# Kernel optimization log

Hardware: AMD Instinct MI355X
Metric: run time of the kernel (lower is better)

## Reference

```python
import jax, jax.numpy as jnp
from jax import lax
import numpy as np

H = W = 32          # feature map size (1024px image / stride 32)
A = 9               # 3 scales x 3 ratios
IOU_THR = 0.5
DN = ('NCHW', 'OIHW', 'NCHW')


def _base_anchors():
    scales = [8.0, 16.0, 32.0]
    ratios = [0.5, 1.0, 2.0]
    rows = []
    for s in scales:
        for r in ratios:
            w = s * np.sqrt(r)
            h = s / np.sqrt(r)
            rows.append([-w / 2, -h / 2, w / 2, h / 2])
    return jnp.asarray(np.array(rows, dtype=np.float32))  # [A,4]


def setup_inputs() -> dict:
    key = jax.random.key(0)
    ks = jax.random.split(key, 4)
    x = jax.random.normal(ks[0], (1, 2048, H, W), jnp.float32)
    # small weight scale keeps exp(dw) in a sane range, like a trained RPN
    conv_w = jax.random.normal(ks[1], (512, 2048, 3, 3), jnp.float32) * 0.01
    conv_b = jnp.zeros((512,), jnp.float32)
    cls_w = jax.random.normal(ks[2], (2 * A, 512, 1, 1), jnp.float32) * 0.01
    cls_b = jnp.zeros((2 * A,), jnp.float32)
    bbox_w = jax.random.normal(ks[3], (4 * A, 512, 1, 1), jnp.float32) * 0.01
    bbox_b = jnp.zeros((4 * A,), jnp.float32)
    return {"x": x, "conv_w": conv_w, "conv_b": conv_b,
            "cls_w": cls_w, "cls_b": cls_b, "bbox_w": bbox_w, "bbox_b": bbox_b}


def _conv(x, w, b, pad):
    y = lax.conv_general_dilated(x, w, (1, 1), pad, dimension_numbers=DN)
    return y + b[None, :, None, None]


def _pairwise_iou(boxes):
    # boxes: [N,4] (x1,y1,x2,y2)
    area = (boxes[:, 2] - boxes[:, 0]) * (boxes[:, 3] - boxes[:, 1])
    lt = jnp.maximum(boxes[:, None, :2], boxes[None, :, :2])
    rb = jnp.minimum(boxes[:, None, 2:], boxes[None, :, 2:])
    wh = jnp.clip(rb - lt, 0.0)
    inter = wh[..., 0] * wh[..., 1]
    union = area[:, None] + area[None, :] - inter
    return inter / jnp.maximum(union, 1e-9)


def _nms_keep(boxes_sorted):
    # boxes sorted by descending score; sequential greedy suppression
    n = boxes_sorted.shape[0]
    iou = _pairwise_iou(boxes_sorted)  # [N,N]
    idx = jnp.arange(n)
    def body(i, keep):
        sup = (iou[i] > IOU_THR) & (idx > i) & keep[i]
        return keep & ~sup
    return lax.fori_loop(0, n, body, jnp.ones((n,), bool))


def _rpn_forward(x, conv_w, conv_b, cls_w, cls_b, bbox_w, bbox_b):
    feat = jax.nn.relu(_conv(x, conv_w, conv_b, 'SAME'))            # [1,512,H,W]
    obj = _conv(feat, cls_w, cls_b, 'VALID')                        # [1,18,H,W]
    deltas = _conv(feat, bbox_w, bbox_b, 'VALID')                   # [1,36,H,W]

    # softmax over the 2 classes (torch view(B,2,-1): first 9 channels = class 0)
    probs = jax.nn.softmax(obj[0].reshape(2, -1), axis=0)[1]        # [A*H*W] anchor-major
    scores = probs.reshape(A, H, W).transpose(1, 2, 0).reshape(-1)  # (pos, anchor) order

    # bbox channel layout: channel = a*4 + coord (0::4 slicing in torch)
    d = deltas[0].reshape(A, 4, H, W).transpose(2, 3, 0, 1).reshape(-1, 4)  # [N,4]

    anchors = jnp.tile(_base_anchors(), (H * W, 1))                 # [N,4], pos*9+a
    aw = anchors[:, 2] - anchors[:, 0]
    ah = anchors[:, 3] - anchors[:, 1]
    cx = anchors[:, 0] + 0.5 * aw
    cy = anchors[:, 1] + 0.5 * ah
    px = cx + d[:, 0] * aw
    py = cy + d[:, 1] * ah
    pw = jnp.exp(d[:, 2]) * aw
    ph = jnp.exp(d[:, 3]) * ah
    boxes = jnp.stack([px - 0.5 * pw, py - 0.5 * ph,
                       px + 0.5 * pw, py + 0.5 * ph], axis=1)       # [N,4]

    order = jnp.argsort(-scores)
    boxes_s = boxes[order]
    scores_s = scores[order]
    keep = _nms_keep(boxes_s)
    final_boxes = jnp.where(keep[:, None], boxes_s, 0.0)
    final_scores = jnp.where(keep, scores_s, 0.0)
    return final_boxes, final_scores


def reference(x, conv_w, conv_b, cls_w, cls_b, bbox_w, bbox_b):
    return _rpn_forward(x, conv_w, conv_b, cls_w, cls_b, bbox_w, bbox_b)
```

## Files before the change

### kernel.cpp

```cpp
#include <hip/hip_runtime.h>
#include <cstdint>
#include <cmath>

#define HH 32
#define WW 32
#define NPX 1024
#define CIN 2048
#define CMID 512
#define NA 9
#define NBOX 9216
#define NWRD 144

typedef double f64x4 __attribute__((ext_vector_type(4)));

#if defined(__HIP_DEVICE_COMPILE__)
#if __has_builtin(__builtin_amdgcn_mfma_f64_16x16x4f64)
#define MFMA64(a, b, c) __builtin_amdgcn_mfma_f64_16x16x4f64((a), (b), (c), 0, 0, 0)
#elif __has_builtin(__builtin_amdgcn_mfma_f64_16x16x4_f64)
#define MFMA64(a, b, c) __builtin_amdgcn_mfma_f64_16x16x4_f64((a), (b), (c), 0, 0, 0)
#endif
#if __has_builtin(__builtin_amdgcn_global_load_lds)
#define HAVE_GLL 1
#endif
#endif

__global__ void k_probe(int* __restrict__ flag) {
#ifdef MFMA64
  const int lane = threadIdx.x & 63;
  const int q = lane >> 4, n16 = lane & 15;
  f64x4 z = {0.0, 0.0, 0.0, 0.0};
  f64x4 d1 = MFMA64((double)(n16 + 1), (n16 == 0) ? 1.0 : 0.0, z);
  f64x4 d2 = MFMA64(1.0, (double)(n16 + 1), z);
  bool ok0 = true, ok1 = true, ok2 = true, ok3 = true;
#pragma unroll
  for (int r = 0; r < 4; ++r) {
    const double rc = (double)(4 * q + r + 1);
    const double rs = (double)(q + 4 * r + 1);
    const double p1 = d1[r], p2 = d2[r];
    const double colv = 4.0 * (double)(n16 + 1);
    ok0 &= (p1 == ((n16 == 0) ? 4.0 * rc : 0.0)) && (p2 == colv);
    ok1 &= (p1 == ((n16 == 0) ? 4.0 * rs : 0.0)) && (p2 == colv);
    ok2 &= (p1 == ((4 * q + r == 0) ? colv : 0.0)) && (p2 == 4.0 * rc);
    ok3 &= (p1 == ((q + 4 * r == 0) ? colv : 0.0)) && (p2 == 4.0 * rs);
  }
  const unsigned long long full = ~0ull;
  int f = 0;
  if (__ballot(ok0) == full) f = 1;
  else if (__ballot(ok1) == full) f = 2;
  else if (__ballot(ok2) == full) f = 3;
  else if (__ballot(ok3) == full) f = 4;
  if (threadIdx.x == 0) *flag = f;
#else
  if (threadIdx.x == 0) *flag = 0;
#endif
}

__global__ __launch_bounds__(256, 2) void k_conv3x3_mfma(
    const float* __restrict__ x, const float* __restrict__ wgt,
    double* __restrict__ partial, int chunk, const int* __restrict__ flag) {
#ifdef MFMA64
  const int f = *flag;
  if (f == 0) return;
  const bool swp = (f >= 3);
  const bool contig = (f == 1) || (f == 3);

  __shared__ double xs[2][8 * 153];
  __shared__ float  wsm[2][4608];
  const int tid = threadIdx.x;
  const int pxt = blockIdx.x;
  const int oct = blockIdx.y;
  const int cz  = blockIdx.z;
  const int h0  = pxt * 2;
  const int oc0 = oct * 64;
  const int cbase = cz * chunk;

  const int wv   = tid >> 6;
  const int lane = tid & 63;
  const int q    = lane >> 4;
  const int n16  = lane & 15;

  f64x4 acc[4];
#pragma unroll
  for (int t = 0; t < 4; ++t) acc[t] = (f64x4){0.0, 0.0, 0.0, 0.0};

  float xreg[5];

#ifdef HAVE_GLL
  int wsrc[5];
#pragma unroll
  for (int m = 0; m < 5; ++m) {
    const int k = wv + 4 * m;
    const int fidx = k * 256 + lane * 4;
    const int oc_l = fidx / 72;
    const int rem  = fidx - oc_l * 72;
    wsrc[m] = (oc0 + oc_l) * 18432 + rem;
  }
#define WISSUE(P, C0)                                                          \
  _Pragma("unroll")                                                            \
  for (int m = 0; m < 5; ++m) {                                                \
    const int k = wv + 4 * m;                                                  \
    if (k < 18) {                                                              \
      __builtin_amdgcn_global_load_lds(                                        \
          (const __attribute__((address_space(1))) void*)(wgt + (size_t)wsrc[m] + (size_t)(C0) * 9), \
          (__attribute__((address_space(3))) void*)(&wsm[P][k * 256]),         \
          16, 0, 0);                                                           \
    }                                                                          \
  }
#define WCOMMIT(P)
#else
  float wreg[18];
#define WISSUE(P, C0)                                                          \
  _Pragma("unroll")                                                            \
  for (int k = 0; k < 18; ++k) {                                               \
    const int idx = tid + k * 256;                                             \
    const int oc_l = idx / 72, rem = idx - oc_l * 72;                          \
    wreg[k] = wgt[(size_t)(oc0 + oc_l) * 18432 + (size_t)(C0) * 9 + rem];      \
  }
#define WCOMMIT(P)                                                             \
  _Pragma("unroll")                                                            \
  for (int k = 0; k < 18; ++k) wsm[P][tid + k * 256] = wreg[k];
#endif

#define XLOAD(C0)                                                              \
  _Pragma("unroll")                                                            \
  for (int k = 0; k < 5; ++k) {                                                \
    const int idx = tid + k * 256;                                             \
    float v = 0.f;                                                             \
    if (idx < 1152) {                                                          \
      const int cc = idx / 144, rem = idx - cc * 144;                          \
      const int r = rem / 36, lcol = rem - r * 36;                             \
      const int grow = h0 - 1 + r, gcol = lcol - 1;                            \
      if ((unsigned)grow < 32u && (unsigned)gcol < 32u)                        \
        v = x[((size_t)((C0) + cc) << 10) + (grow << 5) + gcol];               \
    }                                                                          \
    xreg[k] = v;                                                               \
  }

#define XWRITE(P)                                                              \
  _Pragma("unroll")                                                            \
  for (int k = 0; k < 5; ++k) {                                                \
    const int idx = tid + k * 256;                                             \
    if (idx < 1152) {                                                          \
      const int cc = idx / 144, rem = idx - cc * 144;                          \
      const int r = rem / 36, lcol = rem - r * 36;                             \
      xs[P][cc * 153 + r * 38 + lcol] = (double)xreg[k];                       \
    }                                                                          \
  }

  const int nst = chunk >> 3;
  WISSUE(0, cbase)
  XLOAD(cbase)
  XWRITE(0)
  WCOMMIT(0)
  __syncthreads();

  for (int s = 0; s < nst; ++s) {
    const int p = s & 1;
    if (s + 1 < nst) {
      WISSUE(p ^ 1, cbase + (s + 1) * 8)
      XLOAD(cbase + (s + 1) * 8)
    }
    __builtin_amdgcn_sched_barrier(0);

    const double* xb  = &xs[p][q * 153 + n16];
    const float*  wbq = &wsm[p][((wv << 4) + n16) * 72 + q * 9];

#define CONV_INNER(SWPV)                                                       \
    _Pragma("unroll")                                                          \
    for (int tap = 0; tap < 9; ++tap) {                                        \
      const int dy = tap / 3, dx = tap - 3 * (tap / 3);                        \
      _Pragma("unroll")                                                        \
      for (int ksg = 0; ksg < 2; ++ksg) {                                      \
        const double av = (double)wbq[ksg * 36 + tap];                         \
        const double* xq = xb + ksg * 612;                     \
        _Pragma("unroll")                                                      \
        for (int t = 0; t < 4; ++t) {                                          \
          const double bv = xq[((t >> 1) + dy) * 38 + (t & 1) * 16 + dx];      \
          if (SWPV) acc[t] = MFMA64(bv, av, acc[t]);                           \
          else      acc[t] = MFMA64(av, bv, acc[t]);                           \
        }                                                                      \
      }                                                                        \
    }

    if (swp) { CONV_INNER(true) } else { CONV_INNER(false) }
#undef CONV_INNER

    if (s + 1 < nst) {
      XWRITE(p ^ 1)
      WCOMMIT(p ^ 1)
      __syncthreads();
    }
  }
#undef WISSUE
#undef WCOMMIT
#undef XLOAD
#undef XWRITE
  double* out = partial + (size_t)cz * (CMID * NPX);
#pragma unroll
  for (int t = 0; t < 4; ++t) {
    const int px = ((h0 + (t >> 1)) << 5) + ((t & 1) << 4) + n16;
#pragma unroll
    for (int j = 0; j < 4; ++j) {
      const int row = contig ? ((q << 2) + j) : (q + (j << 2));
      const int oc = oc0 + (wv << 4) + row;
      out[(size_t)oc * NPX + px] = acc[t][j];
    }
  }
#endif
}

__global__ __launch_bounds__(256) void k_conv3x3_valu(
    const float* __restrict__ x, const float* __restrict__ wgt,
    double* __restrict__ partial, int chunk, const int* __restrict__ flag) {
  if (*flag != 0) return;
  __shared__ double xs[8][4][36];
  __shared__ double ws_s[8 * 9 * 66];
  const int tid = threadIdx.x;
  const int pxt = blockIdx.x;
  const int oct = blockIdx.y;
  const int cz  = blockIdx.z;
  const int h0  = pxt * 2;
  const int oc0 = oct * 64;
  const int cbase = cz * chunk;

  const int g   = tid & 15;
  const int ty  = tid >> 4;
  const int r_p = g >> 3;
  const int gc  = (g & 7) * 4;

  double acc[4][4];
#pragma unroll
  for (int a = 0; a < 4; ++a)
#pragma unroll
    for (int b = 0; b < 4; ++b) acc[a][b] = 0.0;

  const int stages = chunk >> 3;
  for (int s = 0; s < stages; ++s) {
    const int c0 = cbase + s * 8;
    __syncthreads();
    for (int idx = tid; idx < 1152; idx += 256) {
      int cc = idx / 144, rem = idx - cc * 144;
      int r = rem / 36, lcol = rem - r * 36;
      int grow = h0 - 1 + r, gcol = lcol - 1;
      float v = 0.f;
      if ((unsigned)grow < 32u && (unsigned)gcol < 32u)
        v = x[((size_t)(c0 + cc) << 10) + (grow << 5) + gcol];
      xs[cc][r][lcol] = (double)v;
    }
    for (int idx = tid; idx < 4608; idx += 256) {
      int oc_l = idx / 72, rem = idx - oc_l * 72;
      int cc = rem / 9, t = rem - cc * 9;
      ws_s[(cc * 9 + t) * 66 + oc_l] =
          (double)wgt[(size_t)(oc0 + oc_l) * 18432 + (size_t)(c0 + cc) * 9 + t];
    }
    __syncthreads();
    for (int cc = 0; cc < 8; ++cc) {
      double xr[3][8];
#pragma unroll
      for (int dy = 0; dy < 3; ++dy) {
        const double* xp = &xs[cc][r_p + dy][gc];
#pragma unroll
        for (int k = 0; k < 8; ++k) xr[dy][k] = xp[k];
      }
#pragma unroll
      for (int t = 0; t < 9; ++t) {
        const int dy = t / 3, dx = t - dy * 3;
        const double* wp = &ws_s[(cc * 9 + t) * 66 + ty * 4];
        const double w0 = wp[0], w1 = wp[1], w2 = wp[2], w3 = wp[3];
#pragma unroll
        for (int i = 0; i < 4; ++i) {
          const double xv = xr[dy][i + dx];
          acc[0][i] += w0 * xv;
          acc[1][i] += w1 * xv;
          acc[2][i] += w2 * xv;
          acc[3][i] += w3 * xv;
        }
      }
    }
  }
  const int pxg = (h0 + r_p) * 32 + gc;
  double* out = partial + (size_t)cz * (CMID * NPX);
#pragma unroll
  for (int j = 0; j < 4; ++j)
#pragma unroll
    for (int i = 0; i < 4; ++i)
      out[(size_t)(oc0 + ty * 4 + j) * NPX + pxg + i] = acc[j][i];
}

__global__ void k_reduce(const double* __restrict__ partial,
                         const float* __restrict__ bias,
                         double* __restrict__ feat, int S) {
  int idx = blockIdx.x * 256 + threadIdx.x;
  double s = (double)bias[idx >> 10];
  for (int z = 0; z < S; ++z) s += partial[(size_t)z * (CMID * NPX) + idx];
  feat[idx] = fmax(s, 0.0);
}

__global__ __launch_bounds__(256) void k_1x1(
    const double* __restrict__ feat,
    const float* __restrict__ cls_w, const float* __restrict__ cls_b,
    const float* __restrict__ bbox_w, const float* __restrict__ bbox_b,
    double* __restrict__ logits) {
  __shared__ float wsh[9 * 512];
  const int px = blockIdx.x * 256 + threadIdx.x;
  const int cg = blockIdx.y;
  for (int idx = threadIdx.x; idx < 9 * 512; idx += 256) {
    int j = idx >> 9, c = idx & 511;
    int ch = cg * 9 + j;
    wsh[idx] = (ch < 18) ? cls_w[(size_t)ch * 512 + c]
                         : bbox_w[(size_t)(ch - 18) * 512 + c];
  }
  __syncthreads();
  double acc[9];
#pragma unroll
  for (int j = 0; j < 9; ++j) acc[j] = 0.0;
  for (int c = 0; c < 512; ++c) {
    const double fv = feat[((size_t)c << 10) + px];
#pragma unroll
    for (int j = 0; j < 9; ++j)
      acc[j] += fv * (double)wsh[(j << 9) + c];
  }
#pragma unroll
  for (int j = 0; j < 9; ++j) {
    const int ch = cg * 9 + j;
    const float bias = (ch < 18) ? cls_b[ch] : bbox_b[ch - 18];
    logits[((size_t)ch << 10) + px] = acc[j] + (double)bias;
  }
}

__global__ void k_score_box(const double* __restrict__ logits,
                            double* __restrict__ scores, double* __restrict__ boxes) {
  int i = blockIdx.x * 256 + threadIdx.x;
  int pos = i / 9, a = i - pos * 9;
  const double* obj = logits;
  const double* dl  = logits + 18 * NPX;
  double l0 = obj[a * NPX + pos], l1 = obj[(9 + a) * NPX + pos];
  double delta = l1 - l0;
  scores[i] = 1.0 / (1.0 + exp(-delta));
  double d0 = dl[(a * 4 + 0) * NPX + pos], d1 = dl[(a * 4 + 1) * NPX + pos];
  double d2 = dl[(a * 4 + 2) * NPX + pos], d3 = dl[(a * 4 + 3) * NPX + pos];
  const double s_arr[3] = {8.0, 16.0, 32.0};
  const double r_arr[3] = {0.5, 1.0, 2.0};
  double sA = s_arr[a / 3], rA = r_arr[a % 3];
  double aw = (double)(float)(sA * sqrt(rA));
  double ah = (double)(float)(sA / sqrt(rA));
  double px_ = d0 * aw, py_ = d1 * ah;
  double pw = exp(d2) * aw, ph = exp(d3) * ah;
  boxes[i * 4 + 0] = px_ - 0.5 * pw;
  boxes[i * 4 + 1] = py_ - 0.5 * ph;
  boxes[i * 4 + 2] = px_ + 0.5 * pw;
  boxes[i * 4 + 3] = py_ + 0.5 * ph;
}

__global__ void k_rank_count(const double* __restrict__ scores, int* __restrict__ rank) {
  __shared__ double sj[256];
  int i  = blockIdx.x * 256 + threadIdx.x;
  int jb = blockIdx.y * 256;
  sj[threadIdx.x] = scores[jb + threadIdx.x];
  __syncthreads();
  double si = scores[i];
  int cnt = 0;
  for (int t = 0; t < 256; ++t) {
    double s = sj[t];
    int j = jb + t;
    cnt += (int)((s > si) || (s == si && j < i));
  }
  if (cnt) atomicAdd(&rank[i], cnt);
}

__global__ void k_scatter(const double* __restrict__ scores, const double* __restrict__ boxes,
                          const int* __restrict__ rank,
                          double* __restrict__ scores_s, double* __restrict__ boxes_s) {
  int i = blockIdx.x * 256 + threadIdx.x;
  int r = rank[i];
  scores_s[r] = scores[i];
  boxes_s[r * 4 + 0] = boxes[i * 4 + 0];
  boxes_s[r * 4 + 1] = boxes[i * 4 + 1];
  boxes_s[r * 4 + 2] = boxes[i * 4 + 2];
  boxes_s[r * 4 + 3] = boxes[i * 4 + 3];
}

__global__ void k_mask(const double* __restrict__ boxes_s, unsigned long long* __restrict__ mask) {
  __shared__ double jb[256][4];
  __shared__ double ib[64][4];
  const int tid = threadIdx.x;
  const int j0 = blockIdx.x * 256;
  const int i0 = blockIdx.y * 64;
  for (int idx = tid; idx < 1024; idx += 256) jb[idx >> 2][idx & 3] = boxes_s[j0 * 4 + idx];
  for (int idx = tid; idx < 256; idx += 256) ib[idx >> 2][idx & 3] = boxes_s[i0 * 4 + idx];
  __syncthreads();
  const int il = tid >> 2;
  const int i  = i0 + il;
  const int wq = blockIdx.x * 4 + (tid & 3);
  const int jlb = (tid & 3) * 64;
  unsigned long long m = 0ull;
  if (wq * 64 + 63 > i) {
    double ix1 = ib[il][0], iy1 = ib[il][1], ix2 = ib[il][2], iy2 = ib[il][3];
    double iarea = (ix2 - ix1) * (iy2 - iy1);
    for (int b = 0; b < 64; ++b) {
      int j = wq * 64 + b;
      double jx1 = jb[jlb + b][0], jy1 = jb[jlb + b][1];
      double jx2 = jb[jlb + b][2], jy2 = jb[jlb + b][3];
      double xx1 = fmax(ix1, jx1), yy1 = fmax(iy1, jy1);
      double xx2 = fmin(ix2, jx2), yy2 = fmin(iy2, jy2);
      double iw = fmax(xx2 - xx1, 0.0), ih = fmax(yy2 - yy1, 0.0);
      double inter = iw * ih;
      double jarea = (jx2 - jx1) * (jy2 - jy1);
      double uni = fmax(iarea + jarea - inter, 1e-9);
      bool sup = inter > 0.5 * uni;
      if (sup && j > i) m |= (1ull << b);
    }
  }
  mask[(size_t)i * NWRD + wq] = m;
}

__global__ void k_nms_scan(const unsigned long long* __restrict__ mask,
                           int* __restrict__ keep) {
  const int l = threadIdx.x & 63;
  unsigned long long r0 = 0ull, r1 = 0ull, r2 = (l < 16) ? 0ull : ~0ull;
  const int w0 = l, w1 = l + 64, w2 = l + 128;
  int prev = -1;
  while (true) {
    int cand = 1 << 30;
    unsigned long long b;
    b = ~r0;
    if (w0 * 64 <= prev) b = (w0 * 64 + 63 <= prev) ? 0ull : (b & (~0ull << (prev + 1 - w0 * 64)));
    if (b) cand = w0 * 64 + __ffsll((long long)b) - 1;
    b = ~r1;
    if (w1 * 64 <= prev) b = (w1 * 64 + 63 <= prev) ? 0ull : (b & (~0ull << (prev + 1 - w1 * 64)));
    if (b) { int c = w1 * 64 + __ffsll((long long)b) - 1; cand = c < cand ? c : cand; }
    b = ~r2;
    if (w2 * 64 <= prev) b = (w2 * 64 + 63 <= prev) ? 0ull : (b & (~0ull << (prev + 1 - w2 * 64)));
    if (b) { int c = w2 * 64 + __ffsll((long long)b) - 1; cand = c < cand ? c : cand; }
#pragma unroll
    for (int off = 32; off; off >>= 1) {
      int o = __shfl_xor(cand, off);
      cand = o < cand ? o : cand;
    }
    if (cand >= NBOX) break;
    const int i = cand;
    if (l == 0) keep[i] = 1;
    r0 |= mask[(size_t)i * NWRD + w0];
    r1 |= mask[(size_t)i * NWRD + w1];
    if (l < 16) r2 |= mask[(size_t)i * NWRD + w2];
    prev = i;
  }
}

__global__ void k_finalize(const double* __restrict__ boxes_s, const double* __restrict__ scores_s,
                           const int* __restrict__ keep, float* __restrict__ out) {
  int r = blockIdx.x * 256 + threadIdx.x;
  int k = keep[r];
  out[r * 4 + 0] = k ? (float)boxes_s[r * 4 + 0] : 0.f;
  out[r * 4 + 1] = k ? (float)boxes_s[r * 4 + 1] : 0.f;
  out[r * 4 + 2] = k ? (float)boxes_s[r * 4 + 2] : 0.f;
  out[r * 4 + 3] = k ? (float)boxes_s[r * 4 + 3] : 0.f;
  out[NBOX * 4 + r] = k ? (float)scores_s[r] : 0.f;
}

static inline size_t alignup(size_t v, size_t a) { return (v + a - 1) & ~(a - 1); }

extern "C" void kernel_launch(void* const* d_in, const int* in_sizes, int n_in,
                              void* d_out, int out_size, void* d_ws, size_t ws_size,
                              hipStream_t stream) {
  const float* x      = (const float*)d_in[0];
  const float* conv_w = (const float*)d_in[1];
  const float* conv_b = (const float*)d_in[2];
  const float* cls_w  = (const float*)d_in[3];
  const float* cls_b  = (const float*)d_in[4];
  const float* bbox_w = (const float*)d_in[5];
  const float* bbox_b = (const float*)d_in[6];
  float* out = (float*)d_out;

  char* ws = (char*)d_ws;
  size_t off = 0;
  int* flag = (int*)(ws + off); off = alignup(off + 256, 256);
  unsigned long long* mask = (unsigned long long*)(ws + off); off = alignup(off + (size_t)NBOX * NWRD * 8, 256);
  double* feat     = (double*)(ws + off); off = alignup(off + (size_t)CMID * NPX * 8, 256);
  double* logits   = (double*)(ws + off); off = alignup(off + (size_t)54 * NPX * 8, 256);
  double* scores   = (double*)(ws + off); off = alignup(off + (size_t)NBOX * 8, 256);
  double* boxes    = (double*)(ws + off); off = alignup(off + (size_t)NBOX * 32, 256);
  double* scores_s = (double*)(ws + off); off = alignup(off + (size_t)NBOX * 8, 256);
  double* boxes_s  = (double*)(ws + off); off = alignup(off + (size_t)NBOX * 32, 256);
  int*   rank      = (int*)(ws + off);    off = alignup(off + (size_t)NBOX * 4, 256);
  int*   keep      = (int*)(ws + off);    off = alignup(off + (size_t)NBOX * 4, 256);
  size_t fixed = off;

  int S = 8;
  while (S > 1 && fixed + (size_t)S * CMID * NPX * 8 > ws_size) S >>= 1;
  double* partial = (double*)(ws + fixed);

  const int chunk = CIN / S;

  hipLaunchKernelGGL(k_probe, dim3(1), dim3(64), 0, stream, flag);
  hipLaunchKernelGGL(k_conv3x3_mfma, dim3(16, 8, S), dim3(256), 0, stream,
                     x, conv_w, partial, chunk, flag);
  hipLaunchKernelGGL(k_conv3x3_valu, dim3(16, 8, S), dim3(256), 0, stream,
                     x, conv_w, partial, chunk, flag);
  hipLaunchKernelGGL(k_reduce, dim3((CMID * NPX) / 256), dim3(256), 0, stream,
                     partial, conv_b, feat, S);
  hipLaunchKernelGGL(k_1x1, dim3(4, 6), dim3(256), 0, stream,
                     feat, cls_w, cls_b, bbox_w, bbox_b, logits);
  hipLaunchKernelGGL(k_score_box, dim3(NBOX / 256), dim3(256), 0, stream,
                     logits, scores, boxes);
  hipMemsetAsync(rank, 0, (size_t)NBOX * 4, stream);
  hipMemsetAsync(keep, 0, (size_t)NBOX * 4, stream);
  hipLaunchKernelGGL(k_rank_count, dim3(36, 36), dim3(256), 0, stream, scores, rank);
  hipLaunchKernelGGL(k_scatter, dim3(NBOX / 256), dim3(256), 0, stream,
                     scores, boxes, rank, scores_s, boxes_s);
  hipLaunchKernelGGL(k_mask, dim3(36, 144), dim3(256), 0, stream, boxes_s, mask);
  hipLaunchKernelGGL(k_nms_scan, dim3(1), dim3(64), 0, stream, mask, keep);
  hipLaunchKernelGGL(k_finalize, dim3(NBOX / 256), dim3(256), 0, stream,
                     boxes_s, scores_s, keep, out);
}
```

Measured before the change: 621.9 us.

## Store conv tiles as float in LDS, raise occupancy, float NMS mask with fallback

The conv kernel now keeps its input tile in LDS as float rather than double, which roughly halves that buffer, and raises the launch-bounds occupancy hint from 2 to 3 blocks per CU. Values are converted to double at MFMA operand load time. The NMS mask kernel computes IoU in float and falls back to a double recomputation only for near-threshold pairs. The two memsets are folded into k_score_box. This trades extra conversion instructions and a possible register-pressure squeeze for lower LDS use, fewer double VALU ops and fewer launches.

After: 788.5 us. 26.8% more time.

```diff
diff --git a/kernel.cpp b/kernel.cpp
--- a/kernel.cpp
+++ b/kernel.cpp
@@ -55,7 +55,7 @@
 #endif
 }
 
-__global__ __launch_bounds__(256, 2) void k_conv3x3_mfma(
+__global__ __launch_bounds__(256, 3) void k_conv3x3_mfma(
     const float* __restrict__ x, const float* __restrict__ wgt,
     double* __restrict__ partial, int chunk, const int* __restrict__ flag) {
 #ifdef MFMA64
@@ -64,8 +64,8 @@
   const bool swp = (f >= 3);
   const bool contig = (f == 1) || (f == 3);
 
-  __shared__ double xs[2][8 * 153];
-  __shared__ float  wsm[2][4608];
+  __shared__ float xs[2][8 * 152];
+  __shared__ float wsm[2][4608];
   const int tid = threadIdx.x;
   const int pxt = blockIdx.x;
   const int oct = blockIdx.y;
@@ -143,7 +143,7 @@
     if (idx < 1152) {                                                          \
       const int cc = idx / 144, rem = idx - cc * 144;                          \
       const int r = rem / 36, lcol = rem - r * 36;                             \
-      xs[P][cc * 153 + r * 38 + lcol] = (double)xreg[k];                       \
+      xs[P][cc * 152 + r * 38 + lcol] = xreg[k];                               \
     }                                                                          \
   }
 
@@ -162,8 +162,8 @@
     }
     __builtin_amdgcn_sched_barrier(0);
 
-    const double* xb  = &xs[p][q * 153 + n16];
-    const float*  wbq = &wsm[p][((wv << 4) + n16) * 72 + q * 9];
+    const float* xb  = &xs[p][q * 152 + n16];
+    const float* wbq = &wsm[p][((wv << 4) + n16) * 72 + q * 9];
 
 #define CONV_INNER(SWPV)                                                       \
     _Pragma("unroll")                                                          \
@@ -172,10 +172,10 @@
       _Pragma("unroll")                                                        \
       for (int ksg = 0; ksg < 2; ++ksg) {                                      \
         const double av = (double)wbq[ksg * 36 + tap];                         \
-        const double* xq = xb + ksg * 612;                     \
+        const float* xq = xb + ksg * 608;                      \
         _Pragma("unroll")                                                      \
         for (int t = 0; t < 4; ++t) {                                          \
-          const double bv = xq[((t >> 1) + dy) * 38 + (t & 1) * 16 + dx];      \
+          const double bv = (double)xq[((t >> 1) + dy) * 38 + (t & 1) * 16 + dx]; \
           if (SWPV) acc[t] = MFMA64(bv, av, acc[t]);                           \
           else      acc[t] = MFMA64(av, bv, acc[t]);                           \
         }                                                                      \
@@ -329,8 +329,11 @@
 }
 
 __global__ void k_score_box(const double* __restrict__ logits,
-                            double* __restrict__ scores, double* __restrict__ boxes) {
+                            double* __restrict__ scores, double* __restrict__ boxes,
+                            int* __restrict__ rank, int* __restrict__ keep) {
   int i = blockIdx.x * 256 + threadIdx.x;
+  rank[i] = 0;
+  keep[i] = 0;
   int pos = i / 9, a = i - pos * 9;
   const double* obj = logits;
   const double* dl  = logits + 18 * NPX;
@@ -381,13 +384,13 @@
 }
 
 __global__ void k_mask(const double* __restrict__ boxes_s, unsigned long long* __restrict__ mask) {
-  __shared__ double jb[256][4];
-  __shared__ double ib[64][4];
+  __shared__ float jb[256][4];
+  __shared__ float ib[64][4];
   const int tid = threadIdx.x;
   const int j0 = blockIdx.x * 256;
   const int i0 = blockIdx.y * 64;
-  for (int idx = tid; idx < 1024; idx += 256) jb[idx >> 2][idx & 3] = boxes_s[j0 * 4 + idx];
-  for (int idx = tid; idx < 256; idx += 256) ib[idx >> 2][idx & 3] = boxes_s[i0 * 4 + idx];
+  for (int idx = tid; idx < 1024; idx += 256) jb[idx >> 2][idx & 3] = (float)boxes_s[j0 * 4 + idx];
+  for (int idx = tid; idx < 256; idx += 256) ib[idx >> 2][idx & 3] = (float)boxes_s[i0 * 4 + idx];
   __syncthreads();
   const int il = tid >> 2;
   const int i  = i0 + il;
@@ -395,19 +398,36 @@
   const int jlb = (tid & 3) * 64;
   unsigned long long m = 0ull;
   if (wq * 64 + 63 > i) {
-    double ix1 = ib[il][0], iy1 = ib[il][1], ix2 = ib[il][2], iy2 = ib[il][3];
-    double iarea = (ix2 - ix1) * (iy2 - iy1);
+    const float ix1 = ib[il][0], iy1 = ib[il][1], ix2 = ib[il][2], iy2 = ib[il][3];
+    const float iarea = (ix2 - ix1) * (iy2 - iy1);
     for (int b = 0; b < 64; ++b) {
-      int j = wq * 64 + b;
-      double jx1 = jb[jlb + b][0], jy1 = jb[jlb + b][1];
-      double jx2 = jb[jlb + b][2], jy2 = jb[jlb + b][3];
-      double xx1 = fmax(ix1, jx1), yy1 = fmax(iy1, jy1);
-      double xx2 = fmin(ix2, jx2), yy2 = fmin(iy2, jy2);
-      double iw = fmax(xx2 - xx1, 0.0), ih = fmax(yy2 - yy1, 0.0);
-      double inter = iw * ih;
-      double jarea = (jx2 - jx1) * (jy2 - jy1);
-      double uni = fmax(iarea + jarea - inter, 1e-9);
-      bool sup = inter > 0.5 * uni;
+      const int j = wq * 64 + b;
+      const float jx1 = jb[jlb + b][0], jy1 = jb[jlb + b][1];
+      const float jx2 = jb[jlb + b][2], jy2 = jb[jlb + b][3];
+      const float xx1 = fmaxf(ix1, jx1), yy1 = fmaxf(iy1, jy1);
+      const float xx2 = fminf(ix2, jx2), yy2 = fminf(iy2, jy2);
+      const float iw = fmaxf(xx2 - xx1, 0.f), ih = fmaxf(yy2 - yy1, 0.f);
+      const float inter = iw * ih;
+      const float jarea = (jx2 - jx1) * (jy2 - jy1);
+      const float uni = fmaxf(iarea + jarea - inter, 1e-9f);
+      const float diff = inter - 0.5f * uni;
+      bool sup;
+      if (fabsf(diff) <= 1e-3f * uni) {
+        const double dix1 = boxes_s[(size_t)i * 4 + 0], diy1 = boxes_s[(size_t)i * 4 + 1];
+        const double dix2 = boxes_s[(size_t)i * 4 + 2], diy2 = boxes_s[(size_t)i * 4 + 3];
+        const double djx1 = boxes_s[(size_t)j * 4 + 0], djy1 = boxes_s[(size_t)j * 4 + 1];
+        const double djx2 = boxes_s[(size_t)j * 4 + 2], djy2 = boxes_s[(size_t)j * 4 + 3];
+        const double dxx1 = fmax(dix1, djx1), dyy1 = fmax(diy1, djy1);
+        const double dxx2 = fmin(dix2, djx2), dyy2 = fmin(diy2, djy2);
+        const double diw = fmax(dxx2 - dxx1, 0.0), dih = fmax(dyy2 - dyy1, 0.0);
+        const double dinter = diw * dih;
+        const double dia = (dix2 - dix1) * (diy2 - diy1);
+        const double dja = (djx2 - djx1) * (djy2 - djy1);
+        const double duni = fmax(dia + dja - dinter, 1e-9);
+        sup = dinter > 0.5 * duni;
+      } else {
+        sup = diff > 0.f;
+      }
       if (sup && j > i) m |= (1ull << b);
     }
   }
@@ -502,9 +522,7 @@
   hipLaunchKernelGGL(k_1x1, dim3(4, 6), dim3(256), 0, stream,
                      feat, cls_w, cls_b, bbox_w, bbox_b, logits);
   hipLaunchKernelGGL(k_score_box, dim3(NBOX / 256), dim3(256), 0, stream,
-                     logits, scores, boxes);
-  hipMemsetAsync(rank, 0, (size_t)NBOX * 4, stream);
-  hipMemsetAsync(keep, 0, (size_t)NBOX * 4, stream);
+                     logits, scores, boxes, rank, keep);
   hipLaunchKernelGGL(k_rank_count, dim3(36, 36), dim3(256), 0, stream, scores, rank);
   hipLaunchKernelGGL(k_scatter, dim3(NBOX / 256), dim3(256), 0, stream,
                      scores, boxes, rank, scores_s, boxes_s);
```
